# Optimization experiments

Hardware: AMD Instinct MI355X
Metric: run time of the kernel (lower is better)

Reference implementation:

```python
import jax, jax.numpy as jnp
import numpy as np

B, H, W = 8, 1024, 1024

SOBEL_X = jnp.array([[-1, 0, 1], [-2, 0, 2], [-1, 0, 1]], jnp.float32).reshape(1, 1, 3, 3)
SOBEL_Y = jnp.array([[-1, -2, -1], [0, 0, 0], [1, 2, 1]], jnp.float32).reshape(1, 1, 3, 3)
LAPLACIAN = jnp.array([[0, -1, 0], [-1, 4, -1], [0, -1, 0]], jnp.float32).reshape(1, 1, 3, 3)
TWO_PI = 2.0 * np.pi


def _conv(x, k, pad):
    return jax.lax.conv_general_dilated(
        x, k, window_strides=(1, 1), padding=[(pad, pad), (pad, pad)],
        dimension_numbers=('NCHW', 'OIHW', 'NCHW'))


def _boundary_mask(mask, w):
    ks = 2 * w + 1
    kernel = jnp.ones((1, 1, ks, ks), jnp.float32)
    s = _conv(mask, kernel, w)
    dilated = (s > 0).astype(jnp.float32)
    eroded = (s >= float(ks * ks)).astype(jnp.float32)
    return jnp.clip(dilated - eroded, 0.0, 1.0)


def _elev_grads(e):
    gx = _conv(e, SOBEL_X, 1)
    gy = _conv(e, SOBEL_Y, 1)
    mag = jnp.sqrt(gx * gx + gy * gy + 1e-8)
    dirn = jnp.arctan2(gy, gx + 1e-8)
    curv = _conv(e, LAPLACIAN, 1)
    return mag, dirn, curv


def _high_freq_mask(h, w):
    ii, jj = jnp.meshgrid(jnp.arange(h, dtype=jnp.float32), jnp.arange(w, dtype=jnp.float32), indexing='ij')
    dist = jnp.sqrt((ii - h // 2) ** 2 + (jj - w // 2) ** 2)
    return (dist > min(h, w) * 0.3).astype(jnp.float32).reshape(1, 1, h, w)


def setup_inputs() -> dict:
    key = jax.random.key(0)
    k1, k2, k3 = jax.random.split(key, 3)
    pred = jax.random.normal(k1, (B, 1, H, W), jnp.float32)
    target = jax.random.normal(k2, (B, 1, H, W), jnp.float32)
    mask = jax.random.randint(k3, (B, 1, H, W), 0, 2).astype(jnp.float32)
    return {'pred_elevation': pred, 'target_elevation': target, 'mask': mask}


def reference(pred_elevation, target_elevation, mask):
    # boundary masks for widths 1..3
    bms = [_boundary_mask(mask, w) for w in (1, 2, 3)]

    # ---- gradient continuity loss ----
    p_mag, p_dir, p_curv = _elev_grads(pred_elevation)
    t_mag, t_dir, t_curv = _elev_grads(target_elevation)
    slope_diff = jnp.abs(p_mag - t_mag)
    dir_diff = jnp.abs(p_dir - t_dir)
    dir_diff = jnp.minimum(dir_diff, TWO_PI - dir_diff)
    curv_diff = jnp.abs(p_curv - t_curv)
    grad_loss = 0.0
    for i, bm in enumerate(bms):
        w_sd = 1.0 if i == 0 else 0.5
        w_cv = 2.0 if i == 0 else 1.0
        grad_loss = grad_loss + w_sd * jnp.mean(slope_diff * bm)
        grad_loss = grad_loss + w_sd * jnp.mean(dir_diff * bm)
        grad_loss = grad_loss + w_cv * jnp.mean(curv_diff * bm)
    grad_loss = grad_loss / len(bms)

    # ---- frequency continuity loss ----
    pf = jnp.fft.fft2(pred_elevation)
    tf = jnp.fft.fft2(target_elevation)
    p_magf, t_magf = jnp.abs(pf), jnp.abs(tf)
    p_ph = jnp.arctan2(pf.imag, pf.real)
    t_ph = jnp.arctan2(tf.imag, tf.real)
    hf = _high_freq_mask(H, W)
    mag_loss = jnp.mean((p_magf * hf - t_magf * hf) ** 2)
    d = p_ph - t_ph
    phase_diff = jnp.arctan2(jnp.sin(d), jnp.cos(d))  # wrap to (-pi, pi]
    phase_loss = jnp.mean((phase_diff * hf) ** 2)
    freq_loss = mag_loss + 2.0 * phase_loss

    # ---- smoothness constraint (width_1 only) ----
    kern9 = jnp.ones((1, 1, 3, 3), jnp.float32) / 9.0
    local_mean = _conv(pred_elevation, kern9, 1)
    local_mean_sq = _conv(pred_elevation ** 2, kern9, 1)
    local_var = jnp.clip(local_mean_sq - local_mean ** 2, 1e-8, None)
    local_std = jnp.sqrt(local_var)
    smooth_loss = jnp.mean(local_std * bms[0])

    # ---- slope continuity (width_1 only) ----
    psx = _conv(p_mag, SOBEL_X, 1)
    psy = _conv(p_mag, SOBEL_Y, 1)
    p_change = jnp.sqrt(psx ** 2 + psy ** 2 + 1e-8)
    tsx = _conv(t_mag, SOBEL_X, 1)
    tsy = _conv(t_mag, SOBEL_Y, 1)
    t_change = jnp.sqrt(tsx ** 2 + tsy ** 2 + 1e-8)
    slope_loss = jnp.mean(jnp.abs(p_change - t_change) * bms[0])

    total = 2.0 * grad_loss + 1.5 * freq_loss + 3.0 * smooth_loss + 2.0 * slope_loss
    return (total, grad_loss, freq_loss, smooth_loss, slope_loss)
```

## Files before the change

### kernel.cpp

```cpp
#include <hip/hip_runtime.h>

#define HW 1024
#define TWO_PI_F 6.28318530717958647692f
#define NSLOT 64

__device__ __forceinline__ float2 cmulf(float2 a, float2 b){
  return make_float2(a.x*b.x - a.y*b.y, a.x*b.y + a.y*b.x);
}
__device__ __forceinline__ float fsqrt(float x){ return __builtin_amdgcn_sqrtf(x); }

__device__ __forceinline__ float fast_atan2f(float y, float x){
  float ax = fabsf(x), ay = fabsf(y);
  float mx = fmaxf(ax, ay), mn = fminf(ax, ay);
  float a  = mn * __builtin_amdgcn_rcpf(fmaxf(mx, 1e-37f));
  float s  = a * a;
  float r  = ((((0.0208351f*s - 0.085133f)*s + 0.180141f)*s - 0.3302995f)*s
              + 0.999866f) * a;
  r = (ay > ax) ? 1.57079632679f - r : r;
  r = (x < 0.f) ? 3.14159265359f - r : r;
  return (y < 0.f) ? -r : r;
}

__device__ __forceinline__ float block_reduce_add_f(float v, float* sc){
  int tid = threadIdx.x;
  #pragma unroll
  for (int o = 32; o > 0; o >>= 1) v += __shfl_down(v, o, 64);
  __syncthreads();
  if ((tid & 63) == 0) sc[tid >> 6] = v;
  __syncthreads();
  return sc[0] + sc[1] + sc[2] + sc[3];
}

__global__ void setup_kernel(double* acc, float2* twg){
  int i = threadIdx.x + blockIdx.x * 256;
  if (i < 5 * NSLOT) acc[i] = 0.0;
  if (i < 512){
    float s, c; sincosf(-TWO_PI_F * (float)i * (1.f/1024.f), &s, &c);
    twg[i] = make_float2(c, s);
  }
}

__global__ __launch_bounds__(256)
void spatial_kernel(const float* __restrict__ pred, const float* __restrict__ targ,
                    const float* __restrict__ mask, double* __restrict__ acc){
  __shared__ float sp[36*37];
  __shared__ float st[36*37];
  __shared__ float smkf[38*39];
  __shared__ unsigned long long mrow[38];
  __shared__ float pmg[34*35];
  __shared__ float tmg[34*35];
  __shared__ float sc[4];

  const int tid = threadIdx.x;
  const int x0 = blockIdx.x << 5, y0 = blockIdx.y << 5;
  const int z = blockIdx.z;
  const size_t ib = (size_t)z * ((size_t)HW * HW);

  for (int i = tid; i < 1296; i += 256){
    int a = i / 36, b = i % 36;
    int gy = y0 - 2 + a, gx = x0 - 2 + b;
    float pv = 0.f, tv = 0.f;
    if ((unsigned)gy < HW && (unsigned)gx < HW){
      size_t idx = ib + (size_t)gy * HW + gx;
      pv = pred[idx]; tv = targ[idx];
    }
    sp[a*37+b] = pv; st[a*37+b] = tv;
  }
  for (int i = tid; i < 1444; i += 256){
    int a = i / 38, b = i % 38;
    int gy = y0 - 3 + a, gx = x0 - 3 + b;
    float v = 0.f;
    if ((unsigned)gy < HW && (unsigned)gx < HW) v = mask[ib + (size_t)gy * HW + gx];
    smkf[a*39+b] = v;
  }
  __syncthreads();

  if (tid < 38){
    unsigned long long w = 0ull;
    #pragma unroll
    for (int x = 0; x < 38; x++)
      w |= (smkf[tid*39 + x] > 0.5f) ? (1ull << x) : 0ull;
    mrow[tid] = w;
  }

  for (int i = tid; i < 1156; i += 256){
    int iy = i / 34, ix = i % 34;
    int gy = y0 - 1 + iy, gx = x0 - 1 + ix;
    float pv = 0.f, tv = 0.f;
    if ((unsigned)gy < HW && (unsigned)gx < HW){
      int o = (iy)*37 + ix;
      float a00=sp[o], a01=sp[o+1], a02=sp[o+2];
      float a10=sp[o+37],           a12=sp[o+39];
      float a20=sp[o+74], a21=sp[o+75], a22=sp[o+76];
      float gxp = (a02 + 2.f*a12 + a22) - (a00 + 2.f*a10 + a20);
      float gyp = (a20 + 2.f*a21 + a22) - (a00 + 2.f*a01 + a02);
      pv = fsqrt(gxp*gxp + gyp*gyp + 1e-8f);
      float b00=st[o], b01=st[o+1], b02=st[o+2];
      float b10=st[o+37],           b12=st[o+39];
      float b20=st[o+74], b21=st[o+75], b22=st[o+76];
      float gxt = (b02 + 2.f*b12 + b22) - (b00 + 2.f*b10 + b20);
      float gyt = (b20 + 2.f*b21 + b22) - (b00 + 2.f*b01 + b02);
      tv = fsqrt(gxt*gxt + gyt*gyt + 1e-8f);
    }
    pmg[iy*35+ix] = pv; tmg[iy*35+ix] = tv;
  }
  __syncthreads();

  const int ty = tid >> 5, tx = tid & 31;
  const int r0 = ty << 2;

  int c1[10], c2[10], c3[10];
  #pragma unroll
  for (int j = 0; j < 10; j++){
    unsigned w = (unsigned)(mrow[r0 + j] >> tx);
    c3[j] = __popc(w & 0x7Fu);
    c2[j] = __popc((w >> 1) & 0x1Fu);
    c1[j] = __popc((w >> 2) & 0x7u);
  }

  float P[3][3], Q[3][3], A[3][3], B[3][3];
  #pragma unroll
  for (int rr = 0; rr < 3; rr++)
    #pragma unroll
    for (int cc = 0; cc < 3; cc++){
      P[rr][cc] = sp[(r0+1+rr)*37 + tx+1+cc];
      Q[rr][cc] = st[(r0+1+rr)*37 + tx+1+cc];
      A[rr][cc] = pmg[(r0+rr)*35 + tx+cc];
      B[rr][cc] = tmg[(r0+rr)*35 + tx+cc];
    }

  float accg = 0.f, accs = 0.f, accl = 0.f;
  #pragma unroll
  for (int k = 0; k < 4; k++){
    if (k){
      #pragma unroll
      for (int cc = 0; cc < 3; cc++){
        P[0][cc]=P[1][cc]; P[1][cc]=P[2][cc]; P[2][cc]=sp[(r0+k+3)*37 + tx+1+cc];
        Q[0][cc]=Q[1][cc]; Q[1][cc]=Q[2][cc]; Q[2][cc]=st[(r0+k+3)*37 + tx+1+cc];
        A[0][cc]=A[1][cc]; A[1][cc]=A[2][cc]; A[2][cc]=pmg[(r0+k+2)*35 + tx+cc];
        B[0][cc]=B[1][cc]; B[1][cc]=B[2][cc]; B[2][cc]=tmg[(r0+k+2)*35 + tx+cc];
      }
    }
    float gxp = (P[0][2]+2.f*P[1][2]+P[2][2]) - (P[0][0]+2.f*P[1][0]+P[2][0]);
    float gyp = (P[2][0]+2.f*P[2][1]+P[2][2]) - (P[0][0]+2.f*P[0][1]+P[0][2]);
    float cvp = 4.f*P[1][1] - P[0][1] - P[1][0] - P[1][2] - P[2][1];
    float gxt = (Q[0][2]+2.f*Q[1][2]+Q[2][2]) - (Q[0][0]+2.f*Q[1][0]+Q[2][0]);
    float gyt = (Q[2][0]+2.f*Q[2][1]+Q[2][2]) - (Q[0][0]+2.f*Q[0][1]+Q[0][2]);
    float cvt = 4.f*Q[1][1] - Q[0][1] - Q[1][0] - Q[1][2] - Q[2][1];

    float sd = fabsf(A[1][1] - B[1][1]);
    float x1 = gxp + 1e-8f, y1 = gyp;
    float x2 = gxt + 1e-8f, y2 = gyt;
    float dd = fabsf(fast_atan2f(y1*x2 - x1*y2, x1*x2 + y1*y2));
    float cd = fabsf(cvp - cvt);

    int s1 = c1[k+2]+c1[k+3]+c1[k+4];
    int s2 = c2[k+1]+c2[k+2]+c2[k+3]+c2[k+4]+c2[k+5];
    int s3 = c3[k]+c3[k+1]+c3[k+2]+c3[k+3]+c3[k+4]+c3[k+5]+c3[k+6];
    float w1 = (s1 > 0 && s1 <  9) ? 1.f : 0.f;
    float w2 = (s2 > 0 && s2 < 25) ? 1.f : 0.f;
    float w3 = (s3 > 0 && s3 < 49) ? 1.f : 0.f;

    accg += (sd + dd) * (w1 + 0.5f*(w2 + w3)) + cd * (2.f*w1 + w2 + w3);

    float s9 = 0.f, s9q = 0.f;
    #pragma unroll
    for (int rr = 0; rr < 3; rr++)
      #pragma unroll
      for (int cc = 0; cc < 3; cc++){ s9 += P[rr][cc]; s9q += P[rr][cc]*P[rr][cc]; }
    float lm = s9 * (1.f/9.f), lq = s9q * (1.f/9.f);
    accs += fsqrt(fmaxf(lq - lm*lm, 1e-8f)) * w1;

    float psx = (A[0][2]+2.f*A[1][2]+A[2][2]) - (A[0][0]+2.f*A[1][0]+A[2][0]);
    float psy = (A[2][0]+2.f*A[2][1]+A[2][2]) - (A[0][0]+2.f*A[0][1]+A[0][2]);
    float pch = fsqrt(psx*psx + psy*psy + 1e-8f);
    float tsx = (B[0][2]+2.f*B[1][2]+B[2][2]) - (B[0][0]+2.f*B[1][0]+B[2][0]);
    float tsy = (B[2][0]+2.f*B[2][1]+B[2][2]) - (B[0][0]+2.f*B[0][1]+B[0][2]);
    float tch = fsqrt(tsx*tsx + tsy*tsy + 1e-8f);
    accl += fabsf(pch - tch) * w1;
  }

  float g  = block_reduce_add_f(accg, sc);
  float sm = block_reduce_add_f(accs, sc);
  float sl = block_reduce_add_f(accl, sc);
  if (tid == 0){
    int slot = (blockIdx.x + blockIdx.y * 7 + z * 13) & (NSLOT - 1);
    atomicAdd(&acc[0*NSLOT + slot], (double)g);
    atomicAdd(&acc[1*NSLOT + slot], (double)sm);
    atomicAdd(&acc[2*NSLOT + slot], (double)sl);
  }
}

__device__ __forceinline__ float lane_xor(float x, int h, int lane){
  int xi = __float_as_int(x);
  int r;
  if (h == 1)       r = __builtin_amdgcn_update_dpp(xi, xi, 0xB1, 0xF, 0xF, true);
  else if (h == 2)  r = __builtin_amdgcn_update_dpp(xi, xi, 0x4E, 0xF, 0xF, true);
  else if (h == 8)  r = __builtin_amdgcn_update_dpp(xi, xi, 0x128, 0xF, 0xF, true);
  else if (h == 4)  r = __builtin_amdgcn_ds_swizzle(xi, 0x101F);
  else if (h == 16) r = __builtin_amdgcn_ds_swizzle(xi, 0x401F);
  else              r = __builtin_amdgcn_ds_bpermute((lane ^ 32) << 2, xi);
  return __int_as_float(r);
}

#define FC 0.70710678118654752f
#define FC1 0.92387953251128676f
#define FS1 0.38268343236508977f

__device__ __forceinline__ void bfly(float2& a, float2& b){
  float tx = b.x, ty = b.y;
  b.x = a.x - tx; b.y = a.y - ty;
  a.x += tx;      a.y += ty;
}
__device__ __forceinline__ void cmul_c(float2& b, float wr, float wi){
  float tx = wr*b.x - wi*b.y, ty = wr*b.y + wi*b.x;
  b.x = tx; b.y = ty;
}
__device__ __forceinline__ void rotmi(float2& b){
  float t = b.x; b.x = b.y; b.y = -t;
}

__device__ __forceinline__ void fft16_reg(float2* v){
  float2 y[16];
  y[0]=v[0];  y[1]=v[8];  y[2]=v[4];  y[3]=v[12];
  y[4]=v[2];  y[5]=v[10]; y[6]=v[6];  y[7]=v[14];
  y[8]=v[1];  y[9]=v[9];  y[10]=v[5]; y[11]=v[13];
  y[12]=v[3]; y[13]=v[11];y[14]=v[7]; y[15]=v[15];
  #pragma unroll
  for (int g = 0; g < 8; g++) bfly(y[2*g], y[2*g+1]);
  #pragma unroll
  for (int g = 0; g < 4; g++){
    int b = 4*g;
    bfly(y[b], y[b+2]);
    rotmi(y[b+3]); bfly(y[b+1], y[b+3]);
  }
  #pragma unroll
  for (int g = 0; g < 2; g++){
    int b = 8*g;
    bfly(y[b], y[b+4]);
    cmul_c(y[b+5],  FC, -FC); bfly(y[b+1], y[b+5]);
    rotmi(y[b+6]);            bfly(y[b+2], y[b+6]);
    cmul_c(y[b+7], -FC, -FC); bfly(y[b+3], y[b+7]);
  }
  bfly(y[0], y[8]);
  cmul_c(y[9],   FC1, -FS1); bfly(y[1], y[9]);
  cmul_c(y[10],  FC,  -FC);  bfly(y[2], y[10]);
  cmul_c(y[11],  FS1, -FC1); bfly(y[3], y[11]);
  rotmi(y[12]);              bfly(y[4], y[12]);
  cmul_c(y[13], -FS1, -FC1); bfly(y[5], y[13]);
  cmul_c(y[14], -FC,  -FC);  bfly(y[6], y[14]);
  cmul_c(y[15], -FC1, -FS1); bfly(y[7], y[15]);
  #pragma unroll
  for (int j = 0; j < 16; j++) v[j] = y[j];
}

__device__ __forceinline__ void fft1024_wave(float2* v, int lane,
                                             const float2* __restrict__ twg){
  #pragma unroll
  for (int s = 0; s < 6; s++){
    const int h = 1 << s;
    const bool up = (lane & h) != 0;
    float2 w = make_float2(1.f, 0.f);
    if (s > 0) w = twg[(lane & (h - 1)) << (9 - s)];
    #pragma unroll
    for (int j = 0; j < 16; j++){
      float ox = lane_xor(v[j].x, h, lane);
      float oy = lane_xor(v[j].y, h, lane);
      float cx = up ? v[j].x : ox;
      float cy = up ? v[j].y : oy;
      float tx, ty;
      if (s == 0){ tx = cx; ty = cy; }
      else { tx = w.x*cx - w.y*cy; ty = w.x*cy + w.y*cx; }
      v[j].x = up ? (ox - tx) : (v[j].x + tx);
      v[j].y = up ? (oy - ty) : (v[j].y + ty);
    }
  }
  float2 wq = twg[lane];
  float2 cur = make_float2(1.f, 0.f);
  #pragma unroll
  for (int j = 1; j < 16; j++){
    cur = cmulf(cur, wq);
    v[j] = cmulf(v[j], cur);
  }
  fft16_reg(v);
}

__global__ __launch_bounds__(512)
void fft_rows_t_kernel(const float* __restrict__ pred, const float* __restrict__ targ,
                       float2* __restrict__ Zt, const float2* __restrict__ twg){
  __shared__ float2 tile[4][64][9];
  const int tid = threadIdx.x;
  const int lane = tid & 63;
  const int w = tid >> 6;
  const int y0 = blockIdx.x << 3;
  const size_t ibase = ((size_t)blockIdx.y * HW + (y0 + w)) * HW;
  const int rb = __brev(lane) >> 26;
  const float4* p4 = (const float4*)(pred + ibase);
  const float4* t4 = (const float4*)(targ + ibase);
  float2 v[16];
  #pragma unroll
  for (int m = 0; m < 4; m++){
    float4 a = p4[4*rb + m];
    float4 b = t4[4*rb + m];
    v[4*m+0] = make_float2(a.x, b.x);
    v[4*m+1] = make_float2(a.y, b.y);
    v[4*m+2] = make_float2(a.z, b.z);
    v[4*m+3] = make_float2(a.w, b.w);
  }
  fft1024_wave(v, lane, twg);
  float2* zb = Zt + (size_t)blockIdx.y * HW * HW + (size_t)blockIdx.x * 8192;
  const int yl = tid & 7, kl = tid >> 3;
  #pragma unroll
  for (int jb = 0; jb < 4; jb++){
    __syncthreads();
    #pragma unroll
    for (int jj = 0; jj < 4; jj++) tile[jj][lane][w] = v[4*jb + jj];
    __syncthreads();
    #pragma unroll
    for (int jj = 0; jj < 4; jj++){
      int k = ((jb << 2) + jj) * 64 + kl;
      zb[k * 8 + yl] = tile[jj][kl][yl];
    }
  }
}

__device__ __forceinline__ void freq_contrib(float2 Zk, float2 Zm, int k1, int k2,
                                             float& ms, float& ps){
  int di = k1 - 512, dj = k2 - 512;
  if (di*di + dj*dj < 94372) return;
  float pr = 0.5f*(Zk.x + Zm.x);
  float pi = 0.5f*(Zk.y - Zm.y);
  float tr = 0.5f*(Zk.y + Zm.y);
  float ti = 0.5f*(Zm.x - Zk.x);
  float p2 = pr*pr + pi*pi;
  float t2 = tr*tr + ti*ti;
  ms += p2 + t2 - 2.f*fsqrt(p2*t2);
  float re = pr*tr + pi*ti;
  float im = pi*tr - pr*ti;
  float pd = fast_atan2f(im, re);
  ps += pd*pd;
}

__global__ __launch_bounds__(256)
void fft_cols2_kernel(const float2* __restrict__ Z, const float2* __restrict__ twg,
                      double* __restrict__ acc){
  __shared__ float2 ex[4][1024];
  const int lane = threadIdx.x & 63;
  const int w = threadIdx.x >> 6;
  const int p = 2 * blockIdx.x + (w >> 1);
  const bool valid = (p <= 512);
  const int r = (w & 1) ? ((1024 - p) & 1023) : p;
  const float2* base = Z + (size_t)blockIdx.y * HW * HW;
  const int rb = __brev(lane) >> 26;

  float2 v[16];
  if (valid){
    const float4* f4 = (const float4*)base;
    #pragma unroll
    for (int s = 0; s < 2; s++){
      size_t o = (size_t)(2*rb + s) * 4096 + (size_t)r * 4;
      #pragma unroll
      for (int q = 0; q < 4; q++){
        float4 x = f4[o + q];
        v[8*s + 2*q]     = make_float2(x.x, x.y);
        v[8*s + 2*q + 1] = make_float2(x.z, x.w);
      }
    }
    fft1024_wave(v, lane, twg);
    #pragma unroll
    for (int j = 0; j < 16; j++) ex[w][lane + (j << 6)] = v[j];
  }
  __syncthreads();
  if (!valid) return;
  const bool self = (p == 0) || (p == 512);
  if ((w & 1) && self) return;

  const float2* pb = ex[w ^ 1];
  float ms = 0.f, ps = 0.f;
  #pragma unroll
  for (int j = 0; j < 16; j++){
    int k = lane + (j << 6);
    float2 zm = pb[(1024 - k) & 1023];
    freq_contrib(v[j], zm, k, r, ms, ps);
  }
  #pragma unroll
  for (int o = 32; o > 0; o >>= 1){
    ms += __shfl_down(ms, o, 64);
    ps += __shfl_down(ps, o, 64);
  }
  if (lane == 0){
    int slot = (r + blockIdx.y * 11) & (NSLOT - 1);
    atomicAdd(&acc[3*NSLOT + slot], (double)ms);
    atomicAdd(&acc[4*NSLOT + slot], (double)ps);
  }
}

__global__ void finalize_kernel(const double* __restrict__ acc, float* __restrict__ out){
  const int t = threadIdx.x;
  double v[5];
  #pragma unroll
  for (int s = 0; s < 5; s++) v[s] = acc[s*NSLOT + t];
  #pragma unroll
  for (int o = 32; o > 0; o >>= 1)
    #pragma unroll
    for (int s = 0; s < 5; s++) v[s] += __shfl_down(v[s], o, 64);
  if (t == 0){
    const double inv = 1.0 / 8388608.0;
    double grad   = v[0] * inv / 3.0;
    double smooth = v[1] * inv;
    double slope  = v[2] * inv;
    double freq   = (v[3] + 2.0 * v[4]) * inv;
    double total  = 2.0*grad + 1.5*freq + 3.0*smooth + 2.0*slope;
    out[0] = (float)total;
    out[1] = (float)grad;
    out[2] = (float)freq;
    out[3] = (float)smooth;
    out[4] = (float)slope;
  }
}

extern "C" void kernel_launch(void* const* d_in, const int* in_sizes, int n_in,
                              void* d_out, int out_size, void* d_ws, size_t ws_size,
                              hipStream_t stream){
  const float* pred = (const float*)d_in[0];
  const float* targ = (const float*)d_in[1];
  const float* mask = (const float*)d_in[2];
  double* acc  = (double*)d_ws;
  float2* twg  = (float2*)((char*)d_ws + 4096);
  float2* Z    = (float2*)((char*)d_ws + 8192);

  setup_kernel<<<2, 256, 0, stream>>>(acc, twg);
  spatial_kernel<<<dim3(32, 32, 8), 256, 0, stream>>>(pred, targ, mask, acc);
  fft_rows_t_kernel<<<dim3(128, 8), 512, 0, stream>>>(pred, targ, Z, twg);
  fft_cols2_kernel<<<dim3(257, 8), 256, 0, stream>>>(Z, twg, acc);
  finalize_kernel<<<1, 64, 0, stream>>>(acc, (float*)d_out);
}
```

Before: 265.8 us.

## Vectorize interior tile loads, alias shared buffers, streamline FFT butterflies and atan2

Interior tiles of the spatial kernel now load pred, target and mask with float4 reads into a padded shared layout. The mask staging buffer shares storage with the magnitude buffers, which needs an extra barrier. The FFT radix-2 stages now apply the twiddle before the lane exchange and combine with one fma, and the per-lane twiddle powers come from a shallower multiply tree instead of a serial chain. The row-FFT transpose uses half as many barrier rounds with a larger tile, and atan2 is reduced to the absolute-value form because callers only need |angle| or its square. Together these cut load instructions, ALU work and syncs, at the cost of more shared memory in the row kernel.

Result: faster. 236.6 us (-11.0%).

```diff
diff --git a/kernel.cpp b/kernel.cpp
--- a/kernel.cpp
+++ b/kernel.cpp
@@ -9,16 +9,15 @@
 }
 __device__ __forceinline__ float fsqrt(float x){ return __builtin_amdgcn_sqrtf(x); }
 
-__device__ __forceinline__ float fast_atan2f(float y, float x){
-  float ax = fabsf(x), ay = fabsf(y);
+__device__ __forceinline__ float fast_atan2_abs(float ay, float x){
+  float ax = fabsf(x);
   float mx = fmaxf(ax, ay), mn = fminf(ax, ay);
   float a  = mn * __builtin_amdgcn_rcpf(fmaxf(mx, 1e-37f));
   float s  = a * a;
   float r  = ((((0.0208351f*s - 0.085133f)*s + 0.180141f)*s - 0.3302995f)*s
               + 0.999866f) * a;
   r = (ay > ax) ? 1.57079632679f - r : r;
-  r = (x < 0.f) ? 3.14159265359f - r : r;
-  return (y < 0.f) ? -r : r;
+  return (x < 0.f) ? 3.14159265359f - r : r;
 }
 
 __device__ __forceinline__ float block_reduce_add_f(float v, float* sc){
@@ -43,35 +42,60 @@
 __global__ __launch_bounds__(256)
 void spatial_kernel(const float* __restrict__ pred, const float* __restrict__ targ,
                     const float* __restrict__ mask, double* __restrict__ acc){
-  __shared__ float sp[36*37];
-  __shared__ float st[36*37];
-  __shared__ float smkf[38*39];
+  __shared__ float sp[36*44];
+  __shared__ float st[36*44];
+  __shared__ float ov[2*34*35];
   __shared__ unsigned long long mrow[38];
-  __shared__ float pmg[34*35];
-  __shared__ float tmg[34*35];
   __shared__ float sc[4];
+  float* const smkf = ov;
+  float* const pmg  = ov;
+  float* const tmg  = ov + 34*35;
 
   const int tid = threadIdx.x;
   const int x0 = blockIdx.x << 5, y0 = blockIdx.y << 5;
   const int z = blockIdx.z;
   const size_t ib = (size_t)z * ((size_t)HW * HW);
-
-  for (int i = tid; i < 1296; i += 256){
-    int a = i / 36, b = i % 36;
-    int gy = y0 - 2 + a, gx = x0 - 2 + b;
-    float pv = 0.f, tv = 0.f;
-    if ((unsigned)gy < HW && (unsigned)gx < HW){
-      size_t idx = ib + (size_t)gy * HW + gx;
-      pv = pred[idx]; tv = targ[idx];
-    }
-    sp[a*37+b] = pv; st[a*37+b] = tv;
-  }
-  for (int i = tid; i < 1444; i += 256){
-    int a = i / 38, b = i % 38;
-    int gy = y0 - 3 + a, gx = x0 - 3 + b;
-    float v = 0.f;
-    if ((unsigned)gy < HW && (unsigned)gx < HW) v = mask[ib + (size_t)gy * HW + gx];
-    smkf[a*39+b] = v;
+  const bool interior = ((unsigned)(blockIdx.x - 1) < 30u) &&
+                        ((unsigned)(blockIdx.y - 1) < 30u);
+
+  if (interior){
+    const float* pb = pred + ib;
+    const float* tb = targ + ib;
+    for (int i = tid; i < 360; i += 256){
+      int a = i / 10, b = i % 10;
+      size_t off = (size_t)(y0 - 2 + a) * HW + (x0 - 4 + 4*b);
+      float4 pv = *(const float4*)(pb + off);
+      float4 tv = *(const float4*)(tb + off);
+      int o = a*44 + 4*b;
+      sp[o]=pv.x; sp[o+1]=pv.y; sp[o+2]=pv.z; sp[o+3]=pv.w;
+      st[o]=tv.x; st[o+1]=tv.y; st[o+2]=tv.z; st[o+3]=tv.w;
+    }
+    const float* mb = mask + ib;
+    for (int i = tid; i < 380; i += 256){
+      int a = i / 10, b = i % 10;
+      size_t off = (size_t)(y0 - 3 + a) * HW + (x0 - 4 + 4*b);
+      float4 v = *(const float4*)(mb + off);
+      int o = a*41 + 4*b;
+      smkf[o]=v.x; smkf[o+1]=v.y; smkf[o+2]=v.z; smkf[o+3]=v.w;
+    }
+  } else {
+    for (int i = tid; i < 1296; i += 256){
+      int a = i / 36, b = i % 36;
+      int gy = y0 - 2 + a, gx = x0 - 2 + b;
+      float pv = 0.f, tv = 0.f;
+      if ((unsigned)gy < HW && (unsigned)gx < HW){
+        size_t idx = ib + (size_t)gy * HW + gx;
+        pv = pred[idx]; tv = targ[idx];
+      }
+      sp[a*44 + b + 2] = pv; st[a*44 + b + 2] = tv;
+    }
+    for (int i = tid; i < 1444; i += 256){
+      int a = i / 38, b = i % 38;
+      int gy = y0 - 3 + a, gx = x0 - 3 + b;
+      float v = 0.f;
+      if ((unsigned)gy < HW && (unsigned)gx < HW) v = mask[ib + (size_t)gy * HW + gx];
+      smkf[a*41 + b + 1] = v;
+    }
   }
   __syncthreads();
 
@@ -79,25 +103,26 @@
     unsigned long long w = 0ull;
     #pragma unroll
     for (int x = 0; x < 38; x++)
-      w |= (smkf[tid*39 + x] > 0.5f) ? (1ull << x) : 0ull;
+      w |= (smkf[tid*41 + 1 + x] > 0.5f) ? (1ull << x) : 0ull;
     mrow[tid] = w;
   }
+  __syncthreads();
 
   for (int i = tid; i < 1156; i += 256){
     int iy = i / 34, ix = i % 34;
     int gy = y0 - 1 + iy, gx = x0 - 1 + ix;
     float pv = 0.f, tv = 0.f;
     if ((unsigned)gy < HW && (unsigned)gx < HW){
-      int o = (iy)*37 + ix;
+      int o = iy*44 + ix + 2;
       float a00=sp[o], a01=sp[o+1], a02=sp[o+2];
-      float a10=sp[o+37],           a12=sp[o+39];
-      float a20=sp[o+74], a21=sp[o+75], a22=sp[o+76];
+      float a10=sp[o+44],           a12=sp[o+46];
+      float a20=sp[o+88], a21=sp[o+89], a22=sp[o+90];
       float gxp = (a02 + 2.f*a12 + a22) - (a00 + 2.f*a10 + a20);
       float gyp = (a20 + 2.f*a21 + a22) - (a00 + 2.f*a01 + a02);
       pv = fsqrt(gxp*gxp + gyp*gyp + 1e-8f);
       float b00=st[o], b01=st[o+1], b02=st[o+2];
-      float b10=st[o+37],           b12=st[o+39];
-      float b20=st[o+74], b21=st[o+75], b22=st[o+76];
+      float b10=st[o+44],           b12=st[o+46];
+      float b20=st[o+88], b21=st[o+89], b22=st[o+90];
       float gxt = (b02 + 2.f*b12 + b22) - (b00 + 2.f*b10 + b20);
       float gyt = (b20 + 2.f*b21 + b22) - (b00 + 2.f*b01 + b02);
       tv = fsqrt(gxt*gxt + gyt*gyt + 1e-8f);
@@ -123,8 +148,8 @@
   for (int rr = 0; rr < 3; rr++)
     #pragma unroll
     for (int cc = 0; cc < 3; cc++){
-      P[rr][cc] = sp[(r0+1+rr)*37 + tx+1+cc];
-      Q[rr][cc] = st[(r0+1+rr)*37 + tx+1+cc];
+      P[rr][cc] = sp[(r0+1+rr)*44 + tx+3+cc];
+      Q[rr][cc] = st[(r0+1+rr)*44 + tx+3+cc];
       A[rr][cc] = pmg[(r0+rr)*35 + tx+cc];
       B[rr][cc] = tmg[(r0+rr)*35 + tx+cc];
     }
@@ -135,8 +160,8 @@
     if (k){
       #pragma unroll
       for (int cc = 0; cc < 3; cc++){
-        P[0][cc]=P[1][cc]; P[1][cc]=P[2][cc]; P[2][cc]=sp[(r0+k+3)*37 + tx+1+cc];
-        Q[0][cc]=Q[1][cc]; Q[1][cc]=Q[2][cc]; Q[2][cc]=st[(r0+k+3)*37 + tx+1+cc];
+        P[0][cc]=P[1][cc]; P[1][cc]=P[2][cc]; P[2][cc]=sp[(r0+k+3)*44 + tx+3+cc];
+        Q[0][cc]=Q[1][cc]; Q[1][cc]=Q[2][cc]; Q[2][cc]=st[(r0+k+3)*44 + tx+3+cc];
         A[0][cc]=A[1][cc]; A[1][cc]=A[2][cc]; A[2][cc]=pmg[(r0+k+2)*35 + tx+cc];
         B[0][cc]=B[1][cc]; B[1][cc]=B[2][cc]; B[2][cc]=tmg[(r0+k+2)*35 + tx+cc];
       }
@@ -151,15 +176,15 @@
     float sd = fabsf(A[1][1] - B[1][1]);
     float x1 = gxp + 1e-8f, y1 = gyp;
     float x2 = gxt + 1e-8f, y2 = gyt;
-    float dd = fabsf(fast_atan2f(y1*x2 - x1*y2, x1*x2 + y1*y2));
+    float dd = fast_atan2_abs(fabsf(y1*x2 - x1*y2), x1*x2 + y1*y2);
     float cd = fabsf(cvp - cvt);
 
     int s1 = c1[k+2]+c1[k+3]+c1[k+4];
     int s2 = c2[k+1]+c2[k+2]+c2[k+3]+c2[k+4]+c2[k+5];
     int s3 = c3[k]+c3[k+1]+c3[k+2]+c3[k+3]+c3[k+4]+c3[k+5]+c3[k+6];
-    float w1 = (s1 > 0 && s1 <  9) ? 1.f : 0.f;
-    float w2 = (s2 > 0 && s2 < 25) ? 1.f : 0.f;
-    float w3 = (s3 > 0 && s3 < 49) ? 1.f : 0.f;
+    float w1 = ((unsigned)(s1 - 1) <  8u) ? 1.f : 0.f;
+    float w2 = ((unsigned)(s2 - 1) < 24u) ? 1.f : 0.f;
+    float w3 = ((unsigned)(s3 - 1) < 48u) ? 1.f : 0.f;
 
     accg += (sd + dd) * (w1 + 0.5f*(w2 + w3)) + cd * (2.f*w1 + w2 + w3);
 
@@ -256,39 +281,64 @@
 
 __device__ __forceinline__ void fft1024_wave(float2* v, int lane,
                                              const float2* __restrict__ twg){
-  #pragma unroll
-  for (int s = 0; s < 6; s++){
+  {
+    const float sgn = (lane & 1) ? -1.f : 1.f;
+    #pragma unroll
+    for (int j = 0; j < 16; j++){
+      float ox = lane_xor(v[j].x, 1, lane);
+      float oy = lane_xor(v[j].y, 1, lane);
+      v[j].x = fmaf(sgn, v[j].x, ox);
+      v[j].y = fmaf(sgn, v[j].y, oy);
+    }
+  }
+  #pragma unroll
+  for (int s = 1; s < 6; s++){
     const int h = 1 << s;
     const bool up = (lane & h) != 0;
-    float2 w = make_float2(1.f, 0.f);
-    if (s > 0) w = twg[(lane & (h - 1)) << (9 - s)];
+    const float2 w = twg[(lane & (h - 1)) << (9 - s)];
+    const float ewx = up ? w.x : 1.f;
+    const float ewy = up ? w.y : 0.f;
+    const float sgn = up ? -1.f : 1.f;
     #pragma unroll
     for (int j = 0; j < 16; j++){
-      float ox = lane_xor(v[j].x, h, lane);
-      float oy = lane_xor(v[j].y, h, lane);
-      float cx = up ? v[j].x : ox;
-      float cy = up ? v[j].y : oy;
-      float tx, ty;
-      if (s == 0){ tx = cx; ty = cy; }
-      else { tx = w.x*cx - w.y*cy; ty = w.x*cy + w.y*cx; }
-      v[j].x = up ? (ox - tx) : (v[j].x + tx);
-      v[j].y = up ? (oy - ty) : (v[j].y + ty);
-    }
-  }
-  float2 wq = twg[lane];
-  float2 cur = make_float2(1.f, 0.f);
-  #pragma unroll
-  for (int j = 1; j < 16; j++){
-    cur = cmulf(cur, wq);
-    v[j] = cmulf(v[j], cur);
-  }
+      float tx = ewx*v[j].x - ewy*v[j].y;
+      float ty = ewx*v[j].y + ewy*v[j].x;
+      float ox = lane_xor(tx, h, lane);
+      float oy = lane_xor(ty, h, lane);
+      v[j].x = fmaf(sgn, tx, ox);
+      v[j].y = fmaf(sgn, ty, oy);
+    }
+  }
+  float2 w1 = twg[lane];
+  float2 w2 = cmulf(w1, w1);
+  float2 w3 = cmulf(w2, w1);
+  float2 w4 = cmulf(w2, w2);
+  float2 w5 = cmulf(w3, w2);
+  float2 w6 = cmulf(w3, w3);
+  float2 w7 = cmulf(w4, w3);
+  float2 w8 = cmulf(w4, w4);
+  v[1]  = cmulf(v[1],  w1);
+  v[2]  = cmulf(v[2],  w2);
+  v[3]  = cmulf(v[3],  w3);
+  v[4]  = cmulf(v[4],  w4);
+  v[5]  = cmulf(v[5],  w5);
+  v[6]  = cmulf(v[6],  w6);
+  v[7]  = cmulf(v[7],  w7);
+  v[8]  = cmulf(v[8],  w8);
+  v[9]  = cmulf(cmulf(v[9],  w8), w1);
+  v[10] = cmulf(cmulf(v[10], w8), w2);
+  v[11] = cmulf(cmulf(v[11], w8), w3);
+  v[12] = cmulf(cmulf(v[12], w8), w4);
+  v[13] = cmulf(cmulf(v[13], w8), w5);
+  v[14] = cmulf(cmulf(v[14], w8), w6);
+  v[15] = cmulf(cmulf(v[15], w8), w7);
   fft16_reg(v);
 }
 
 __global__ __launch_bounds__(512)
 void fft_rows_t_kernel(const float* __restrict__ pred, const float* __restrict__ targ,
                        float2* __restrict__ Zt, const float2* __restrict__ twg){
-  __shared__ float2 tile[4][64][9];
+  __shared__ float2 tile[8][64][9];
   const int tid = threadIdx.x;
   const int lane = tid & 63;
   const int w = tid >> 6;
@@ -311,14 +361,14 @@
   float2* zb = Zt + (size_t)blockIdx.y * HW * HW + (size_t)blockIdx.x * 8192;
   const int yl = tid & 7, kl = tid >> 3;
   #pragma unroll
-  for (int jb = 0; jb < 4; jb++){
+  for (int jb = 0; jb < 2; jb++){
     __syncthreads();
     #pragma unroll
-    for (int jj = 0; jj < 4; jj++) tile[jj][lane][w] = v[4*jb + jj];
+    for (int jj = 0; jj < 8; jj++) tile[jj][lane][w] = v[8*jb + jj];
     __syncthreads();
     #pragma unroll
-    for (int jj = 0; jj < 4; jj++){
-      int k = ((jb << 2) + jj) * 64 + kl;
+    for (int jj = 0; jj < 8; jj++){
+      int k = ((jb << 3) + jj) * 64 + kl;
       zb[k * 8 + yl] = tile[jj][kl][yl];
     }
   }
@@ -337,7 +387,7 @@
   ms += p2 + t2 - 2.f*fsqrt(p2*t2);
   float re = pr*tr + pi*ti;
   float im = pi*tr - pr*ti;
-  float pd = fast_atan2f(im, re);
+  float pd = fast_atan2_abs(fabsf(im), re);
   ps += pd*pd;
 }
 
```
